# Performance work log

Measured on AMD Instinct MI355X. Metric: run time of the kernel, lower is better.

Reference implementation:

```python
import jax, jax.numpy as jnp
import numpy as np

MERGE_COEFF = 0.5  # fixed beta-merge coefficient (init arg)


def setup_inputs() -> dict:
    key = jax.random.key(0)
    k1, k2, k3, k4 = jax.random.split(key, 4)
    N, M, H = 8192, 8192, 512
    s = 1.0 / np.sqrt(H)
    return {
        "features": jax.random.normal(k1, (N, H), dtype=jnp.float32),
        "memory_features": jax.random.normal(k2, (M, H), dtype=jnp.float32),
        "Wq": jax.random.normal(k3, (H, H), dtype=jnp.float32) * s,
        "bq": jnp.zeros((H,), dtype=jnp.float32),
        "Wk": jax.random.normal(k4, (H, H), dtype=jnp.float32) * s,
        "bk": jnp.zeros((H,), dtype=jnp.float32),
    }


def reference(features, memory_features, Wq, bq, Wk, bk):
    tau = 1.0
    # torch nn.Linear: y = x @ W.T + b
    q = features @ Wq.T + bq                 # [N, H]
    k = memory_features @ Wk.T + bk          # [M, H]
    attn = jax.nn.softmax((q @ k.T) / tau, axis=-1)  # [N, M]
    augment = attn @ memory_features          # [N, H]
    c = MERGE_COEFF
    return c * features + (1.0 - c) * augment
```

## Files before the change

kernel.cpp:

```cpp
#include <hip/hip_runtime.h>


typedef _Float16 half8 __attribute__((ext_vector_type(8)));
typedef _Float16 half4 __attribute__((ext_vector_type(4)));
typedef float floatx4 __attribute__((ext_vector_type(4)));

#define MFMA16(a, b, c) __builtin_amdgcn_mfma_f32_16x16x32_f16((a), (b), (c), 0, 0, 0)

static constexpr int H = 512;
static constexpr int NROWS = 8192;

__device__ __forceinline__ void dma16(half8* lds_dst, const void* g_src) {
    __builtin_amdgcn_global_load_lds(
        (const __attribute__((address_space(1))) unsigned int*)g_src,
        (__attribute__((address_space(3))) unsigned int*)lds_dst,
        16, 0, 0);
}

__global__ void castall_kernel(const float* __restrict__ F, const float* __restrict__ Mem,
                               const float* __restrict__ wq, const float* __restrict__ wk,
                               _Float16* __restrict__ f16, _Float16* __restrict__ m16,
                               _Float16* __restrict__ wq16, _Float16* __restrict__ wk16) {
    size_t i4 = (size_t)(blockIdx.x * 256 + threadIdx.x) * 4;
    const float* src; _Float16* dst; size_t off;
    if (i4 < 4194304ull)       { src = F;   dst = f16;  off = i4; }
    else if (i4 < 8388608ull)  { src = Mem; dst = m16;  off = i4 - 4194304ull; }
    else if (i4 < 8650752ull)  { src = wq;  dst = wq16; off = i4 - 8388608ull; }
    else                       { src = wk;  dst = wk16; off = i4 - 8650752ull; }
    float4 v = *(const float4*)&src[off];
    half4 h;
    h[0] = (_Float16)v.x; h[1] = (_Float16)v.y; h[2] = (_Float16)v.z; h[3] = (_Float16)v.w;
    *(half4*)&dst[off] = h;
}

__global__ void packv_kernel(const _Float16* __restrict__ m16, half8* __restrict__ vp) {
    const int kb = blockIdx.x;
    const int t  = threadIdx.x;
    const int c = t & 15, db = t >> 4;
    const _Float16* base = m16 + (size_t)kb * 32 * H + db * 16 + c;
#pragma unroll
    for (int g = 0; g < 4; ++g) {
        half8 v;
#pragma unroll
        for (int j = 0; j < 8; ++j) v[j] = base[(size_t)(g * 8 + j) * H];
        vp[(size_t)kb * 2048 + db * 64 + g * 16 + c] = v;
    }
}

__global__ __launch_bounds__(256, 4)
void proj_kernel(const _Float16* __restrict__ Xq, const _Float16* __restrict__ Wq16,
                 const float* __restrict__ bq, _Float16* __restrict__ oq,
                 const _Float16* __restrict__ Xk, const _Float16* __restrict__ Wk16,
                 const float* __restrict__ bk, _Float16* __restrict__ ok) {
    const _Float16* X16 = blockIdx.z ? Xk : Xq;
    const _Float16* W16 = blockIdx.z ? Wk16 : Wq16;
    const float*    bias = blockIdx.z ? bk : bq;
    _Float16*       out = blockIdx.z ? ok : oq;

    const int lane = threadIdx.x & 63;
    const int wave = threadIdx.x >> 6;
    const int row0 = blockIdx.x * 128 + wave * 32;
    const int col0 = blockIdx.y * 64;
    const int lr = lane & 15, lq = lane >> 4;

    floatx4 acc[2][4];
#pragma unroll
    for (int rt = 0; rt < 2; ++rt)
#pragma unroll
        for (int nt = 0; nt < 4; ++nt) { acc[rt][nt][0] = 0.f; acc[rt][nt][1] = 0.f; acc[rt][nt][2] = 0.f; acc[rt][nt][3] = 0.f; }

    const half8* ar0 = (const half8*)(X16 + (size_t)(row0 + lr) * H) + lq;
    const half8* ar1 = (const half8*)(X16 + (size_t)(row0 + 16 + lr) * H) + lq;
    const half8* wbase = (const half8*)W16;

#pragma unroll
    for (int kk = 0; kk < 16; ++kk) {
        half8 a0 = ar0[kk * 4];
        half8 a1 = ar1[kk * 4];
#pragma unroll
        for (int nt = 0; nt < 4; ++nt) {
            half8 bf = wbase[(size_t)(col0 + nt * 16 + lr) * 64 + kk * 4 + lq];
            acc[0][nt] = MFMA16(a0, bf, acc[0][nt]);
            acc[1][nt] = MFMA16(a1, bf, acc[1][nt]);
        }
    }
#pragma unroll
    for (int rt = 0; rt < 2; ++rt)
#pragma unroll
        for (int nt = 0; nt < 4; ++nt) {
            int col = col0 + nt * 16 + lr;
            float b = bias[col];
#pragma unroll
            for (int r = 0; r < 4; ++r) {
                int row = row0 + rt * 16 + lq * 4 + r;
                out[(size_t)row * H + col] = (_Float16)(acc[rt][nt][r] + b);
            }
        }
}

__global__ __launch_bounds__(512, 2)
void flash_kernel(const _Float16* __restrict__ q16, const _Float16* __restrict__ k16,
                  const half8* __restrict__ vp, _Float16* __restrict__ opart,
                  float* __restrict__ mpart, float* __restrict__ lpart) {
    __shared__ half8 klds[2][2048];
    __shared__ half8 vlds[2][2048];
    __shared__ _Float16 plds[2][128 * 36];
    __shared__ float alds[2][128];
    __shared__ float llds[128];
    __shared__ int flagw[2][8];

    const int tid = threadIdx.x;
    const int lane = tid & 63;
    const int wave = tid >> 6;
    const int rbk = blockIdx.x >> 2;
    const int slice = blockIdx.x & 3;
    const int row0 = rbk * 128;
    const int lr = lane & 15, lq = lane >> 4;

    int koff[4];
#pragma unroll
    for (int i = 0; i < 4; ++i) {
        int d = tid + i * 512;
        int c = d >> 10, kk = (d >> 6) & 15, g = (d >> 4) & 3, cc = d & 15;
        koff[i] = c * 8192 + cc * 512 + kk * 32 + g * 8;
    }

    const half8* qrow = (const half8*)(q16 + (size_t)(row0 + wave * 16 + lr) * H);
    half8 qf[16];
#pragma unroll
    for (int kk = 0; kk < 16; ++kk) qf[kk] = qrow[kk * 4 + lq];

    floatx4 o[8][4];
#pragma unroll
    for (int rb = 0; rb < 8; ++rb)
#pragma unroll
        for (int f = 0; f < 4; ++f) { o[rb][f][0] = 0.f; o[rb][f][1] = 0.f; o[rb][f][2] = 0.f; o[rb][f][3] = 0.f; }
    float m[4], l[4];
#pragma unroll
    for (int r = 0; r < 4; ++r) { m[r] = -1e30f; l[r] = 0.f; }

    {
        const int kt0 = slice * 64;
        const _Float16* ksrc0 = k16 + (size_t)kt0 * 16384;
        const half8* vsrc0 = vp + (size_t)kt0 * 2048;
#pragma unroll
        for (int i = 0; i < 4; ++i) dma16(&klds[0][tid + i * 512], ksrc0 + koff[i]);
#pragma unroll
        for (int i = 0; i < 4; ++i) dma16(&vlds[0][tid + i * 512], &vsrc0[tid + i * 512]);
        const _Float16* ksrc1 = k16 + (size_t)(kt0 + 1) * 16384;
#pragma unroll
        for (int i = 0; i < 4; ++i) dma16(&klds[1][tid + i * 512], ksrc1 + koff[i]);
    }

    for (int tt = 0; tt < 64; ++tt) {
        const int b = tt & 1;

        asm volatile("s_waitcnt vmcnt(8) lgkmcnt(0)" ::: "memory");
        __builtin_amdgcn_s_barrier();

        if (tt > 0) {
            const int q1 = b ^ 1;
#pragma unroll
            for (int rb = 0; rb < 8; ++rb) {
                if (flagw[q1][rb]) {
                    float a0 = alds[q1][rb * 16 + lq * 4 + 0];
                    float a1 = alds[q1][rb * 16 + lq * 4 + 1];
                    float a2 = alds[q1][rb * 16 + lq * 4 + 2];
                    float a3 = alds[q1][rb * 16 + lq * 4 + 3];
#pragma unroll
                    for (int f = 0; f < 4; ++f) {
                        o[rb][f][0] *= a0; o[rb][f][1] *= a1;
                        o[rb][f][2] *= a2; o[rb][f][3] *= a3;
                    }
                }
            }
            __builtin_amdgcn_s_setprio(1);
            half8 vf[4];
#pragma unroll
            for (int f = 0; f < 4; ++f) vf[f] = vlds[q1][(wave * 4 + f) * 64 + lane];
#pragma unroll
            for (int rb = 0; rb < 8; ++rb) {
                half8 pfr = *(const half8*)&plds[q1][(rb * 16 + lr) * 36 + lq * 8];
#pragma unroll
                for (int f = 0; f < 4; ++f) o[rb][f] = MFMA16(pfr, vf[f], o[rb][f]);
            }
            __builtin_amdgcn_s_setprio(0);
        }

        __builtin_amdgcn_s_setprio(1);
        floatx4 s0 = {0.f, 0.f, 0.f, 0.f}, s1 = {0.f, 0.f, 0.f, 0.f};
#pragma unroll
        for (int kk = 0; kk < 16; ++kk) {
            s0 = MFMA16(qf[kk], klds[b][kk * 64 + lane], s0);
            s1 = MFMA16(qf[kk], klds[b][1024 + kk * 64 + lane], s1);
        }
        __builtin_amdgcn_s_setprio(0);

        float tm[4]; int trig = 0;
#pragma unroll
        for (int r = 0; r < 4; ++r) {
            tm[r] = fmaxf(s0[r], s1[r]);
            trig |= (tm[r] > m[r] + 10.f) ? 1 : 0;
        }
        const int trigany = __any(trig) ? 1 : 0;
        if (lane == 0) flagw[b][wave] = trigany;
        if (trigany) {
            float al[4];
#pragma unroll
            for (int r = 0; r < 4; ++r) {
                float mx = tm[r];
                mx = fmaxf(mx, __shfl_xor(mx, 1));
                mx = fmaxf(mx, __shfl_xor(mx, 2));
                mx = fmaxf(mx, __shfl_xor(mx, 4));
                mx = fmaxf(mx, __shfl_xor(mx, 8));
                float mn = (mx > m[r] + 10.f) ? mx : m[r];
                al[r] = __expf(m[r] - mn);
                m[r] = mn;
                l[r] *= al[r];
            }
            if (lr == 0) {
#pragma unroll
                for (int r = 0; r < 4; ++r) alds[b][wave * 16 + lq * 4 + r] = al[r];
            }
        }

#pragma unroll
        for (int r = 0; r < 4; ++r) {
            float p0 = __expf(s0[r] - m[r]);
            float p1 = __expf(s1[r] - m[r]);
            l[r] += p0 + p1;
            plds[b][(wave * 16 + lq * 4 + r) * 36 + lr]      = (_Float16)p0;
            plds[b][(wave * 16 + lq * 4 + r) * 36 + 16 + lr] = (_Float16)p1;
        }

        asm volatile("s_waitcnt lgkmcnt(0)" ::: "memory");
        __builtin_amdgcn_s_barrier();

        {
            int vt = tt + 1; if (vt > 63) vt = 63;
            int kt2 = tt + 2; if (kt2 > 63) kt2 = 63;
            const half8* vsrc = vp + (size_t)(slice * 64 + vt) * 2048;
#pragma unroll
            for (int i = 0; i < 4; ++i) dma16(&vlds[(tt + 1) & 1][tid + i * 512], &vsrc[tid + i * 512]);
            const _Float16* ksrc = k16 + (size_t)(slice * 64 + kt2) * 16384;
#pragma unroll
            for (int i = 0; i < 4; ++i) dma16(&klds[b][tid + i * 512], ksrc + koff[i]);
        }
    }

    asm volatile("s_waitcnt lgkmcnt(0)" ::: "memory");
    {
#pragma unroll
        for (int rb = 0; rb < 8; ++rb) {
            if (flagw[1][rb]) {
                float a0 = alds[1][rb * 16 + lq * 4 + 0];
                float a1 = alds[1][rb * 16 + lq * 4 + 1];
                float a2 = alds[1][rb * 16 + lq * 4 + 2];
                float a3 = alds[1][rb * 16 + lq * 4 + 3];
#pragma unroll
                for (int f = 0; f < 4; ++f) {
                    o[rb][f][0] *= a0; o[rb][f][1] *= a1;
                    o[rb][f][2] *= a2; o[rb][f][3] *= a3;
                }
            }
        }
        __builtin_amdgcn_s_setprio(1);
        half8 vf[4];
#pragma unroll
        for (int f = 0; f < 4; ++f) vf[f] = vlds[1][(wave * 4 + f) * 64 + lane];
#pragma unroll
        for (int rb = 0; rb < 8; ++rb) {
            half8 pfr = *(const half8*)&plds[1][(rb * 16 + lr) * 36 + lq * 8];
#pragma unroll
            for (int f = 0; f < 4; ++f) o[rb][f] = MFMA16(pfr, vf[f], o[rb][f]);
        }
        __builtin_amdgcn_s_setprio(0);
    }

#pragma unroll
    for (int r = 0; r < 4; ++r) {
        float lv = l[r];
        lv += __shfl_xor(lv, 1); lv += __shfl_xor(lv, 2);
        lv += __shfl_xor(lv, 4); lv += __shfl_xor(lv, 8);
        l[r] = lv;
    }
    if (lr == 0) {
#pragma unroll
        for (int r = 0; r < 4; ++r) {
            int row = wave * 16 + lq * 4 + r;
            llds[row] = l[r];
            mpart[slice * NROWS + row0 + row] = m[r];
            lpart[slice * NROWS + row0 + row] = l[r];
        }
    }
    __syncthreads();

    _Float16* ob = opart + (size_t)slice * NROWS * H;
#pragma unroll
    for (int rb = 0; rb < 8; ++rb) {
#pragma unroll
        for (int rr = 0; rr < 4; ++rr) {
            float linv = 1.0f / llds[rb * 16 + lq * 4 + rr];
            size_t row = row0 + rb * 16 + lq * 4 + rr;
#pragma unroll
            for (int f = 0; f < 4; ++f)
                ob[row * H + wave * 64 + f * 16 + lr] = (_Float16)(o[rb][f][rr] * linv);
        }
    }
}

__global__ void merge_kernel(const _Float16* __restrict__ opart, const float* __restrict__ mpart,
                             const float* __restrict__ lpart, const float* __restrict__ F,
                             float* __restrict__ out) {
    int gid = blockIdx.x * 256 + threadIdx.x;
    size_t idx4 = (size_t)gid * 4;
    int row = (int)(idx4 >> 9);
    float m0 = mpart[row], m1 = mpart[NROWS + row], m2 = mpart[2 * NROWS + row], m3 = mpart[3 * NROWS + row];
    float ms = fmaxf(fmaxf(m0, m1), fmaxf(m2, m3));
    float w0 = __expf(m0 - ms) * lpart[row];
    float w1 = __expf(m1 - ms) * lpart[NROWS + row];
    float w2 = __expf(m2 - ms) * lpart[2 * NROWS + row];
    float w3 = __expf(m3 - ms) * lpart[3 * NROWS + row];
    float rdenom = 1.0f / (w0 + w1 + w2 + w3);
    size_t stride = (size_t)NROWS * H;
    half4 o0 = *(const half4*)&opart[idx4];
    half4 o1 = *(const half4*)&opart[stride + idx4];
    half4 o2 = *(const half4*)&opart[2 * stride + idx4];
    half4 o3 = *(const half4*)&opart[3 * stride + idx4];
    float4 Fv = *(const float4*)&F[idx4];
    float4 res;
    res.x = 0.5f * Fv.x + 0.5f * ((w0 * (float)o0[0] + w1 * (float)o1[0] + w2 * (float)o2[0] + w3 * (float)o3[0]) * rdenom);
    res.y = 0.5f * Fv.y + 0.5f * ((w0 * (float)o0[1] + w1 * (float)o1[1] + w2 * (float)o2[1] + w3 * (float)o3[1]) * rdenom);
    res.z = 0.5f * Fv.z + 0.5f * ((w0 * (float)o0[2] + w1 * (float)o1[2] + w2 * (float)o2[2] + w3 * (float)o3[2]) * rdenom);
    res.w = 0.5f * Fv.w + 0.5f * ((w0 * (float)o0[3] + w1 * (float)o1[3] + w2 * (float)o2[3] + w3 * (float)o3[3]) * rdenom);
    *(float4*)&out[idx4] = res;
}

extern "C" void kernel_launch(void* const* d_in, const int* in_sizes, int n_in,
                              void* d_out, int out_size, void* d_ws, size_t ws_size,
                              hipStream_t stream) {
    const float* F   = (const float*)d_in[0];
    const float* Mem = (const float*)d_in[1];
    const float* Wq  = (const float*)d_in[2];
    const float* bq  = (const float*)d_in[3];
    const float* Wk  = (const float*)d_in[4];
    const float* bk  = (const float*)d_in[5];
    float* out = (float*)d_out;

    char* ws = (char*)d_ws;
    _Float16* q16   = (_Float16*)(ws);
    _Float16* k16   = (_Float16*)(ws + (8ull << 20));
    half8*    vp    = (half8*)(ws + (16ull << 20));
    _Float16* opart = (_Float16*)(ws + (24ull << 20));
    _Float16* f16F  = (_Float16*)(ws + (24ull << 20));
    _Float16* m16   = (_Float16*)(ws + (32ull << 20));
    float*    mpart = (float*)(ws + (56ull << 20));
    float*    lpart = (float*)(ws + (56ull << 20) + (128ull << 10));
    _Float16* wq16  = (_Float16*)(ws + (57ull << 20));
    _Float16* wk16  = (_Float16*)(ws + (57ull << 20) + (512ull << 10));

    castall_kernel<<<8704, 256, 0, stream>>>(F, Mem, Wq, Wk, f16F, m16, wq16, wk16);
    packv_kernel<<<256, 512, 0, stream>>>(m16, vp);
    proj_kernel<<<dim3(64, 8, 2), 256, 0, stream>>>(f16F, wq16, bq, q16, m16, wk16, bk, k16);
    flash_kernel<<<256, 512, 0, stream>>>(q16, k16, vp, opart, mpart, lpart);
    merge_kernel<<<4096, 256, 0, stream>>>(opart, mpart, lpart, F, out);
}
```

Before: 334.7 us.

## Fuse V packing into cast kernel and load V fragments directly into registers

The separate packv launch is merged into the cast kernel: extra blocks read fp32 memory features directly, convert them and write the packed V layout. Inside the flash kernel, the V double-buffer in LDS is removed. Each wave now loads its V fragments from global memory (L2) into registers one iteration ahead of their use, and an initial wait and barrier is added for the K prefetch. This saves one launch and halves the LDS footprint, which may allow higher occupancy, but the direct global loads of V can expose latency inside the main loop.

```diff
diff --git a/kernel.cpp b/kernel.cpp
--- a/kernel.cpp
+++ b/kernel.cpp
@@ -17,33 +17,34 @@
         16, 0, 0);
 }
 
-__global__ void castall_kernel(const float* __restrict__ F, const float* __restrict__ Mem,
-                               const float* __restrict__ wq, const float* __restrict__ wk,
-                               _Float16* __restrict__ f16, _Float16* __restrict__ m16,
-                               _Float16* __restrict__ wq16, _Float16* __restrict__ wk16) {
-    size_t i4 = (size_t)(blockIdx.x * 256 + threadIdx.x) * 4;
-    const float* src; _Float16* dst; size_t off;
-    if (i4 < 4194304ull)       { src = F;   dst = f16;  off = i4; }
-    else if (i4 < 8388608ull)  { src = Mem; dst = m16;  off = i4 - 4194304ull; }
-    else if (i4 < 8650752ull)  { src = wq;  dst = wq16; off = i4 - 8388608ull; }
-    else                       { src = wk;  dst = wk16; off = i4 - 8650752ull; }
-    float4 v = *(const float4*)&src[off];
-    half4 h;
-    h[0] = (_Float16)v.x; h[1] = (_Float16)v.y; h[2] = (_Float16)v.z; h[3] = (_Float16)v.w;
-    *(half4*)&dst[off] = h;
-}
-
-__global__ void packv_kernel(const _Float16* __restrict__ m16, half8* __restrict__ vp) {
-    const int kb = blockIdx.x;
-    const int t  = threadIdx.x;
-    const int c = t & 15, db = t >> 4;
-    const _Float16* base = m16 + (size_t)kb * 32 * H + db * 16 + c;
-#pragma unroll
-    for (int g = 0; g < 4; ++g) {
+__global__ void castpack_kernel(const float* __restrict__ F, const float* __restrict__ Mem,
+                                const float* __restrict__ wq, const float* __restrict__ wk,
+                                _Float16* __restrict__ f16, _Float16* __restrict__ m16,
+                                _Float16* __restrict__ wq16, _Float16* __restrict__ wk16,
+                                half8* __restrict__ vp) {
+    if (blockIdx.x < 8704) {
+        size_t i4 = (size_t)(blockIdx.x * 256 + threadIdx.x) * 4;
+        const float* src; _Float16* dst; size_t off;
+        if (i4 < 4194304ull)       { src = F;   dst = f16;  off = i4; }
+        else if (i4 < 8388608ull)  { src = Mem; dst = m16;  off = i4 - 4194304ull; }
+        else if (i4 < 8650752ull)  { src = wq;  dst = wq16; off = i4 - 8388608ull; }
+        else                       { src = wk;  dst = wk16; off = i4 - 8650752ull; }
+        float4 v = *(const float4*)&src[off];
+        half4 h;
+        h[0] = (_Float16)v.x; h[1] = (_Float16)v.y; h[2] = (_Float16)v.z; h[3] = (_Float16)v.w;
+        *(half4*)&dst[off] = h;
+    } else {
+        int cid = (blockIdx.x - 8704) * 256 + threadIdx.x;
+        int kb  = cid >> 11;
+        int rem = cid & 2047;
+        int db  = rem >> 6;
+        int gc  = rem & 63;
+        int g   = gc >> 4, c = gc & 15;
+        const float* src = Mem + (size_t)(kb * 32 + g * 8) * H + db * 16 + c;
         half8 v;
 #pragma unroll
-        for (int j = 0; j < 8; ++j) v[j] = base[(size_t)(g * 8 + j) * H];
-        vp[(size_t)kb * 2048 + db * 64 + g * 16 + c] = v;
+        for (int j = 0; j < 8; ++j) v[j] = (_Float16)src[(size_t)j * H];
+        vp[cid] = v;
     }
 }
 
@@ -103,7 +104,6 @@
                   const half8* __restrict__ vp, _Float16* __restrict__ opart,
                   float* __restrict__ mpart, float* __restrict__ lpart) {
     __shared__ half8 klds[2][2048];
-    __shared__ half8 vlds[2][2048];
     __shared__ _Float16 plds[2][128 * 36];
     __shared__ float alds[2][128];
     __shared__ float llds[128];
@@ -138,19 +138,19 @@
     float m[4], l[4];
 #pragma unroll
     for (int r = 0; r < 4; ++r) { m[r] = -1e30f; l[r] = 0.f; }
+    half8 vf[4];
 
     {
         const int kt0 = slice * 64;
         const _Float16* ksrc0 = k16 + (size_t)kt0 * 16384;
-        const half8* vsrc0 = vp + (size_t)kt0 * 2048;
 #pragma unroll
         for (int i = 0; i < 4; ++i) dma16(&klds[0][tid + i * 512], ksrc0 + koff[i]);
-#pragma unroll
-        for (int i = 0; i < 4; ++i) dma16(&vlds[0][tid + i * 512], &vsrc0[tid + i * 512]);
         const _Float16* ksrc1 = k16 + (size_t)(kt0 + 1) * 16384;
 #pragma unroll
         for (int i = 0; i < 4; ++i) dma16(&klds[1][tid + i * 512], ksrc1 + koff[i]);
     }
+    asm volatile("s_waitcnt vmcnt(4) lgkmcnt(0)" ::: "memory");
+    __builtin_amdgcn_s_barrier();
 
     for (int tt = 0; tt < 64; ++tt) {
         const int b = tt & 1;
@@ -175,9 +175,6 @@
                 }
             }
             __builtin_amdgcn_s_setprio(1);
-            half8 vf[4];
-#pragma unroll
-            for (int f = 0; f < 4; ++f) vf[f] = vlds[q1][(wave * 4 + f) * 64 + lane];
 #pragma unroll
             for (int rb = 0; rb < 8; ++rb) {
                 half8 pfr = *(const half8*)&plds[q1][(rb * 16 + lr) * 36 + lq * 8];
@@ -185,6 +182,12 @@
                 for (int f = 0; f < 4; ++f) o[rb][f] = MFMA16(pfr, vf[f], o[rb][f]);
             }
             __builtin_amdgcn_s_setprio(0);
+        }
+
+        {
+            const half8* vsrc = vp + (size_t)(slice * 64 + tt) * 2048 + wave * 256 + lane;
+#pragma unroll
+            for (int f = 0; f < 4; ++f) vf[f] = vsrc[f * 64];
         }
 
         __builtin_amdgcn_s_setprio(1);
@@ -237,11 +240,7 @@
         __builtin_amdgcn_s_barrier();
 
         {
-            int vt = tt + 1; if (vt > 63) vt = 63;
             int kt2 = tt + 2; if (kt2 > 63) kt2 = 63;
-            const half8* vsrc = vp + (size_t)(slice * 64 + vt) * 2048;
-#pragma unroll
-            for (int i = 0; i < 4; ++i) dma16(&vlds[(tt + 1) & 1][tid + i * 512], &vsrc[tid + i * 512]);
             const _Float16* ksrc = k16 + (size_t)(slice * 64 + kt2) * 16384;
 #pragma unroll
             for (int i = 0; i < 4; ++i) dma16(&klds[b][tid + i * 512], ksrc + koff[i]);
@@ -265,9 +264,6 @@
             }
         }
         __builtin_amdgcn_s_setprio(1);
-        half8 vf[4];
-#pragma unroll
-        for (int f = 0; f < 4; ++f) vf[f] = vlds[1][(wave * 4 + f) * 64 + lane];
 #pragma unroll
         for (int rb = 0; rb < 8; ++rb) {
             half8 pfr = *(const half8*)&plds[1][(rb * 16 + lr) * 36 + lq * 8];
@@ -359,8 +355,7 @@
     _Float16* wq16  = (_Float16*)(ws + (57ull << 20));
     _Float16* wk16  = (_Float16*)(ws + (57ull << 20) + (512ull << 10));
 
-    castall_kernel<<<8704, 256, 0, stream>>>(F, Mem, Wq, Wk, f16F, m16, wq16, wk16);
-    packv_kernel<<<256, 512, 0, stream>>>(m16, vp);
+    castpack_kernel<<<10752, 256, 0, stream>>>(F, Mem, Wq, Wk, f16F, m16, wq16, wk16, vp);
     proj_kernel<<<dim3(64, 8, 2), 256, 0, stream>>>(f16F, wq16, bq, q16, m16, wk16, bk, k16);
     flash_kernel<<<256, 512, 0, stream>>>(q16, k16, vp, opart, mpart, lpart);
     merge_kernel<<<4096, 256, 0, stream>>>(opart, mpart, lpart, F, out);
```

After: 355.3 us. 6.1% more time.
